# Kernel optimization log

Hardware: AMD Instinct MI355X
Metric: run time of the kernel (lower is better)

## Reference

```python
import jax, jax.numpy as jnp
import numpy as np

E, M, T, H, V = 512, 1024, 1024, 512, 10000
B, S, L = 16, 80, 200
K = 10  # pooling kernel


def avgpool2d(x, k):
    # torch AvgPool2d(k) on a 3D tensor [B, S, C]: pools over (S, C) with stride k, floor mode
    b, s, c = x.shape
    return x[:, :(s // k) * k, :(c // k) * k].reshape(b, s // k, k, c // k, k).mean(axis=(2, 4))


def lstm(x, h0, c0, Wih, Whh, bih, bhh):
    # torch single-layer LSTM, gate order (i, f, g, o); x: [B, T, H]
    def step(carry, xt):
        h, c = carry
        g = xt @ Wih.T + h @ Whh.T + bih + bhh  # [B, 4H]
        i, f, gg, o = jnp.split(g, 4, axis=-1)
        c = jax.nn.sigmoid(f) * c + jax.nn.sigmoid(i) * jnp.tanh(gg)
        h = jax.nn.sigmoid(o) * jnp.tanh(c)
        return (h, c), h
    (hT, cT), ys = jax.lax.scan(step, (h0, c0), jnp.swapaxes(x, 0, 1))
    return jnp.swapaxes(ys, 0, 1), (hT, cT)


def attend(emb, feats, lens, Ws, bs, hdim):
    # additive score: Linear(cat(emb, feat)) = emb@We.T + feat@Wf.T + b, masked softmax over valid feats
    we, wf = Ws[:, :hdim], Ws[:, hdim:]
    scores = emb @ we.T + jnp.swapaxes(feats @ wf.T, 1, 2) + bs  # [B, S, L]
    mask = jnp.arange(feats.shape[1])[None, None, :] < lens[:, None, None]
    w = jax.nn.softmax(jnp.where(mask, scores, -jnp.inf), axis=-1)
    return jnp.einsum('bsl,blf->bsf', w, feats)


def setup_inputs():
    key = jax.random.key(0)
    ks = jax.random.split(key, 30)
    n = lambda k, shape: jax.random.normal(k, shape, dtype=jnp.float32)
    p = lambda k, shape: 0.02 * jax.random.normal(k, shape, dtype=jnp.float32)
    inp = {
        'mfeat': n(ks[0], (B, L, M)),
        'tfeat': n(ks[1], (B, L, T)),
        'att_motion': n(ks[2], (B, S, M)),
        'att_tempo': n(ks[3], (B, S, T)),
        'embeddings': n(ks[4], (B, S, E)),
        'motion_batch_lens': jax.random.randint(ks[5], (B,), 100, L + 1, dtype=jnp.int32),
        'temp_batch_lens': jax.random.randint(ks[6], (B,), 100, L + 1, dtype=jnp.int32),
        'seq_batch_lens': jnp.full((B,), S, dtype=jnp.int32),
        'Wm': p(ks[7], (M, M)), 'bm': p(ks[8], (M,)),
        'Wt': p(ks[9], (T, T)), 'bt': p(ks[10], (T,)),
        'Wmm': p(ks[11], (H, E + T + M)), 'bmm': p(ks[12], (H,)),
        'Wli': p(ks[13], (H, T // K + M // K)), 'bli': p(ks[14], (H,)),
        'Wih': p(ks[15], (4 * H, H)), 'Whh': p(ks[16], (4 * H, H)),
        'bih': p(ks[17], (4 * H,)), 'bhh': p(ks[18], (4 * H,)),
        'Wsm': p(ks[19], (1, H + M)), 'bsm': p(ks[20], (1,)),
        'Wst': p(ks[21], (1, H + T)), 'bst': p(ks[22], (1,)),
        'Wo': p(ks[23], (V, H + T + M)), 'bo': p(ks[24], (V,)),
    }
    return inp


def reference(mfeat, tfeat, att_motion, att_tempo, embeddings,
              motion_batch_lens, temp_batch_lens, seq_batch_lens,
              Wm, bm, Wt, bt, Wmm, bmm, Wli, bli,
              Wih, Whh, bih, bhh, Wsm, bsm, Wst, bst, Wo, bo):
    # self-gated feature transforms
    temp_mout = att_motion @ Wm.T + bm
    temp_tout = att_tempo @ Wt.T + bt
    temp_mout = temp_mout * jax.nn.softmax(temp_mout, axis=-1)
    temp_tout = temp_tout * jax.nn.softmax(temp_tout, axis=-1)
    # multimodal fusion (dropout = identity in eval)
    mm_inp = jnp.concatenate((embeddings, temp_tout, temp_mout), axis=2)
    mm_out = mm_inp @ Wmm.T + bmm  # [B, S, H]
    # pooled init sequence -> LSTM init hidden
    mean_feat = jnp.concatenate((avgpool2d(att_tempo, K), avgpool2d(att_motion, K)), axis=2)
    m0 = mean_feat @ Wli.T + bli  # [B, S//K, H]
    z = jnp.zeros((att_motion.shape[0], H), dtype=mm_out.dtype)
    _, (h0, c0) = lstm(m0, z, z, Wih, Whh, bih, bhh)
    out, _ = lstm(mm_out, h0, c0, Wih, Whh, bih, bhh)
    act = jnp.tanh(out)
    # ragged additive attention over variable-length video features
    att_m2 = attend(act, mfeat, motion_batch_lens, Wsm, bsm, H)
    att_t2 = attend(act, tfeat, temp_batch_lens, Wst, bst, H)
    final = jnp.concatenate((act, att_t2, att_m2), axis=2) @ Wo.T + bo
    return jax.nn.log_softmax(final, axis=2)
```

## Files before the change

kernel.cpp:

```cpp
#include <hip/hip_runtime.h>
#include <hip/hip_bf16.h>
#include <math.h>


typedef __bf16 bf16x8 __attribute__((ext_vector_type(8)));
typedef float f32x4 __attribute__((ext_vector_type(4)));
typedef unsigned short u16x8 __attribute__((ext_vector_type(8)));

__device__ inline unsigned short f2b(float f){
  union { float f; unsigned u; } v; v.f = f;
  unsigned u = v.u;
  u += 0x7fff + ((u >> 16) & 1);
  return (unsigned short)(u >> 16);
}
__device__ inline float b2f(unsigned short u){
  union { unsigned u; float f; } v; v.u = (unsigned)u << 16; return v.f;
}
__device__ inline float sigm(float x){ return 1.f/(1.f + __expf(-x)); }
__device__ inline float tanh_fast(float x){
  float e = __expf(2.f*x);
  return 1.f - 2.f/(e + 1.f);
}
__device__ inline float wred_max(float v){ for (int o=32;o;o>>=1) v = fmaxf(v, __shfl_xor(v,o)); return v; }
__device__ inline float wred_sum(float v){ for (int o=32;o;o>>=1) v += __shfl_xor(v,o); return v; }

__device__ inline float bred_max(float v, float* sm){
  v = wred_max(v);
  int w = threadIdx.x >> 6;
  if ((threadIdx.x & 63) == 0) sm[w] = v;
  __syncthreads();
  v = fmaxf(fmaxf(sm[0], sm[1]), fmaxf(sm[2], sm[3]));
  __syncthreads();
  return v;
}
__device__ inline float bred_sum(float v, float* sm){
  v = wred_sum(v);
  int w = threadIdx.x >> 6;
  if ((threadIdx.x & 63) == 0) sm[w] = v;
  __syncthreads();
  v = sm[0] + sm[1] + sm[2] + sm[3];
  __syncthreads();
  return v;
}

#define GLOAD_LDS16(g, l) __builtin_amdgcn_global_load_lds( \
    (const __attribute__((address_space(1))) void*)(g), \
    (__attribute__((address_space(3))) void*)(l), 16, 0, 0)

__global__ void zero_kernel(int* p, int n){
  int i = blockIdx.x*64 + threadIdx.x;
  if (i < n) p[i] = 0;
}

__global__ void cvt7_kernel(
    const float* __restrict__ attm, const float* __restrict__ attt,
    const float* __restrict__ Wm,   const float* __restrict__ Wt,
    const float* __restrict__ Wmm,  const float* __restrict__ Wih,
    const float* __restrict__ emb,
    unsigned short* __restrict__ attm_bf, unsigned short* __restrict__ attt_bf,
    unsigned short* __restrict__ Wm_bf,   unsigned short* __restrict__ Wt_bf,
    unsigned short* __restrict__ Wmm_bf,  unsigned short* __restrict__ Wih_bf,
    unsigned short* __restrict__ mm_inp_bf)
{
  int i = blockIdx.x*256 + threadIdx.x;
  const float* s; unsigned short* d; int o;
  if (i < 458752){
    if (i < 163840){ s = attm; d = attm_bf; o = i; }
    else if (i < 327680){ s = attt; d = attt_bf; o = i - 163840; }
    else { s = Wm; d = Wm_bf; o = i - 327680; }
  } else if (i < 753664){
    if (i < 589824){ s = Wt; d = Wt_bf; o = i - 458752; }
    else { s = Wmm; d = Wmm_bf; o = i - 589824; }
  } else {
    if (i < 884736){ s = Wih; d = Wih_bf; o = i - 753664; }
    else { s = emb; d = mm_inp_bf; o = i - 884736; }
  }
  f32x4 a = ((const f32x4*)s)[(size_t)o*2];
  f32x4 b = ((const f32x4*)s)[(size_t)o*2+1];
  u16x8 v;
  v[0]=f2b(a[0]); v[1]=f2b(a[1]); v[2]=f2b(a[2]); v[3]=f2b(a[3]);
  v[4]=f2b(b[0]); v[5]=f2b(b[1]); v[6]=f2b(b[2]); v[7]=f2b(b[3]);
  if (i >= 884736){
    int row = o >> 6, c8 = (o & 63) << 3;
    *(u16x8*)&d[(size_t)row*2560 + c8] = v;
  } else {
    ((u16x8*)d)[o] = v;
  }
}

__device__ __forceinline__ void gemm_body(
    const unsigned short* __restrict__ A, const unsigned short* __restrict__ B,
    const float* __restrict__ bias1, const float* __restrict__ bias2,
    float* __restrict__ C, unsigned short* __restrict__ Cbf, int N, int K,
    unsigned short* lA, unsigned short* lB, int r0, int n0)
{
  int tid = threadIdx.x;
  int w = tid >> 6, lane = tid & 63;
  int wr = (w >> 1) << 6, wc = (w & 1) << 6;
  int lm = lane & 15, lq = lane >> 4;
  f32x4 acc[4][4] = {};

  int row0 = tid >> 2, row1 = (tid + 256) >> 2, cc = (tid & 3) << 3;
  const unsigned short* Ag0 = A + (size_t)(r0 + row0)*K + cc;
  const unsigned short* Ag1 = A + (size_t)(r0 + row1)*K + cc;
  int br0 = n0 + row0; if (br0 >= N) br0 = N - 1;
  int br1 = n0 + row1; if (br1 >= N) br1 = N - 1;
  const unsigned short* Bg0 = B + (size_t)br0*K + cc;
  const unsigned short* Bg1 = B + (size_t)br1*K + cc;
  unsigned lb0 = (unsigned)(tid & ~63) * 8;
  unsigned lb1 = 2048 + lb0;

  for (int k0 = 0; k0 < K; k0 += 32){
    GLOAD_LDS16(Ag0 + k0, &lA[lb0]);
    GLOAD_LDS16(Ag1 + k0, &lA[lb1]);
    GLOAD_LDS16(Bg0 + k0, &lB[lb0]);
    GLOAD_LDS16(Bg1 + k0, &lB[lb1]);
    __syncthreads();
    bf16x8 af[4], bfr[4];
#pragma unroll
    for (int i=0;i<4;i++){
      af[i]  = *(const bf16x8*)&lA[(wr + i*16 + lm)*32 + lq*8];
      bfr[i] = *(const bf16x8*)&lB[(wc + i*16 + lm)*32 + lq*8];
    }
#pragma unroll
    for (int i=0;i<4;i++)
#pragma unroll
      for (int j=0;j<4;j++)
        acc[i][j] = __builtin_amdgcn_mfma_f32_16x16x32_bf16(af[i], bfr[j], acc[i][j], 0, 0, 0);
    __syncthreads();
  }
#pragma unroll
  for (int i=0;i<4;i++){
    int rbase = r0 + wr + i*16 + lq*4;
#pragma unroll
    for (int j=0;j<4;j++){
      int n = n0 + wc + j*16 + lm;
      if (n < N){
        float bv = (bias1 ? bias1[n] : 0.f) + (bias2 ? bias2[n] : 0.f);
        if (Cbf){
#pragma unroll
          for (int rr=0;rr<4;rr++)
            Cbf[(size_t)(rbase + rr)*N + n] = f2b(acc[i][j][rr] + bv);
        } else {
#pragma unroll
          for (int rr=0;rr<4;rr++)
            C[(size_t)(rbase + rr)*N + n] = acc[i][j][rr] + bv;
        }
      }
    }
  }
}

__global__ __launch_bounds__(256) void gemm_bb_kernel(
    const unsigned short* __restrict__ A, const unsigned short* __restrict__ B,
    const float* __restrict__ bias1, const float* __restrict__ bias2,
    float* __restrict__ C, unsigned short* __restrict__ Cbf, int N, int K)
{
  __shared__ unsigned short lA[128*32];
  __shared__ unsigned short lB[128*32];
  gemm_body(A, B, bias1, bias2, C, Cbf, N, K, lA, lB, blockIdx.x << 7, blockIdx.y << 7);
}

__global__ __launch_bounds__(256) void gemm_bb2_kernel(
    const unsigned short* __restrict__ A0, const unsigned short* __restrict__ B0,
    const float* __restrict__ b0, float* __restrict__ C0,
    const unsigned short* __restrict__ A1, const unsigned short* __restrict__ B1,
    const float* __restrict__ b1, float* __restrict__ C1, int N, int K)
{
  __shared__ unsigned short lA[128*32];
  __shared__ unsigned short lB[128*32];
  if (blockIdx.z == 0) gemm_body(A0, B0, b0, nullptr, C0, nullptr, N, K, lA, lB, blockIdx.x << 7, blockIdx.y << 7);
  else                 gemm_body(A1, B1, b1, nullptr, C1, nullptr, N, K, lA, lB, blockIdx.x << 7, blockIdx.y << 7);
}

__global__ __launch_bounds__(256) void gemm_x12_kernel(
    const unsigned short* __restrict__ m0_bf, const unsigned short* __restrict__ mmo_bf,
    const unsigned short* __restrict__ Wih_bf,
    const float* __restrict__ bih, const float* __restrict__ bhh,
    float* __restrict__ X1, float* __restrict__ X2)
{
  __shared__ unsigned short lA[128*32];
  __shared__ unsigned short lB[128*32];
  if (blockIdx.x == 0)
    gemm_body(m0_bf, Wih_bf, bih, bhh, X1, nullptr, 2048, 512, lA, lB, 0, blockIdx.y << 7);
  else
    gemm_body(mmo_bf, Wih_bf, bih, bhh, X2, nullptr, 2048, 512, lA, lB, (blockIdx.x - 1) << 7, blockIdx.y << 7);
}

__global__ __launch_bounds__(256) void rowsmx2_kernel(const float* __restrict__ X0,
    const float* __restrict__ X1, unsigned short* __restrict__ out)
{
  __shared__ float sm[4];
  int bx = blockIdx.x, tid = threadIdx.x;
  int row = (bx < 1280) ? bx : bx - 1280;
  const float* xr = ((bx < 1280) ? X0 : X1) + (size_t)row * 1024;
  int ooff = (bx < 1280) ? 1536 : 512;
  float x[4];
#pragma unroll
  for (int j=0;j<4;j++) x[j] = xr[j*256 + tid];
  float m = fmaxf(fmaxf(x[0],x[1]), fmaxf(x[2],x[3]));
  m = bred_max(m, sm);
  float s = 0.f;
#pragma unroll
  for (int j=0;j<4;j++) s += __expf(x[j]-m);
  s = bred_sum(s, sm);
  float inv = 1.f / s;
  unsigned short* o = out + (size_t)row*2560 + ooff;
#pragma unroll
  for (int j=0;j<4;j++) o[j*256 + tid] = f2b(x[j] * (__expf(x[j]-m) * inv));
}

__global__ __launch_bounds__(256) void m0fused_kernel(
    const float* __restrict__ tempo, const float* __restrict__ motion,
    const float* __restrict__ Wli, const float* __restrict__ bli,
    unsigned short* __restrict__ m0_bf)
{
  __shared__ float rowv[204];
  int bx = blockIdx.x, tid = threadIdx.x;
  int b = bx >> 3, s = bx & 7;
  if (tid < 204){
    int c = tid;
    const float* src = (c < 102) ? (tempo  + ((size_t)(b*80 + s*10))*1024 + c*10)
                                 : (motion + ((size_t)(b*80 + s*10))*1024 + (c-102)*10);
    float acc = 0.f;
    for (int r=0;r<10;r++){
      const float* p = src + (size_t)r*1024;
#pragma unroll
      for (int cc=0;cc<10;cc++) acc += p[cc];
    }
    rowv[c] = acc * 0.01f;
  }
  __syncthreads();
  for (int c = tid; c < 512; c += 256){
    const float* w = Wli + (size_t)c*204;
    float acc = bli[c];
    for (int k=0;k<204;k++) acc += rowv[k]*w[k];
    m0_bf[(size_t)bx*512 + c] = f2b(acc);
  }
}

#define LSTM_NBLK 32
#define HP 520

__global__ __launch_bounds__(256) void lstm_fused_kernel(
    const float* __restrict__ X1, const float* __restrict__ X2,
    const float* __restrict__ Whh,
    unsigned long long* __restrict__ hb0, unsigned long long* __restrict__ hb1,
    unsigned short* __restrict__ finalA_bf,
    int* __restrict__ bar,
    const float* __restrict__ Wo, unsigned short* __restrict__ Wo_bf,
    const float* __restrict__ mfeat, const float* __restrict__ tfeat,
    const float* __restrict__ Wsm, const float* __restrict__ Wst,
    float* __restrict__ f_m, float* __restrict__ f_t)
{
  __shared__ unsigned short w_lds[64*HP];
  __shared__ unsigned short h_lds[16*HP];
  __shared__ float gb[4][16][16];
  __shared__ unsigned short hstage[16][16];
  int tid = threadIdx.x, j = blockIdx.x;

  if (j >= LSTM_NBLK){
    int hb = j - LSTM_NBLK;
    int lane = tid & 63;
    int wv = hb*4 + (tid >> 6);
    for (int r = wv; r < 6400; r += 896){
      const float* a = (r < 3200) ? (mfeat + (size_t)r*1024) : (tfeat + (size_t)(r-3200)*1024);
      const float* wvec = (r < 3200) ? (Wsm + 512) : (Wst + 512);
      float acc = 0.f;
      for (int c = lane; c < 1024; c += 64) acc += a[c]*wvec[c];
      acc = wred_sum(acc);
      if (lane == 0){ if (r < 3200) f_m[r] = acc; else f_t[r-3200] = acc; }
      __builtin_amdgcn_s_sleep(32);
    }
    const f32x4* wp = (const f32x4*)Wo;
    for (int ch = hb*256 + tid; ch < 3200000; ch += 224*256){
      f32x4 a = __builtin_nontemporal_load(wp + (size_t)ch*2);
      f32x4 b = __builtin_nontemporal_load(wp + (size_t)ch*2 + 1);
      u16x8 o;
      o[0]=f2b(a[0]); o[1]=f2b(a[1]); o[2]=f2b(a[2]); o[3]=f2b(a[3]);
      o[4]=f2b(b[0]); o[5]=f2b(b[1]); o[6]=f2b(b[2]); o[7]=f2b(b[3]);
      ((u16x8*)Wo_bf)[ch] = o;
      __builtin_amdgcn_s_sleep(127);
    }
    return;
  }

  int j16 = j*16;
  int lane = tid & 63, w = tid >> 6;
  int lm = lane & 15, lq = lane >> 4;

  for (int i = 0; i < 16; i++){
    int ch = tid + i*256;
    int r = ch >> 6, c8 = (ch & 63) << 3;
    int grow = (r >> 4)*512 + j16 + (r & 15);
    const float* s = Whh + (size_t)grow*512 + c8;
    f32x4 a = ((const f32x4*)s)[0], b = ((const f32x4*)s)[1];
    u16x8 o;
    o[0]=f2b(a[0]); o[1]=f2b(a[1]); o[2]=f2b(a[2]); o[3]=f2b(a[3]);
    o[4]=f2b(b[0]); o[5]=f2b(b[1]); o[6]=f2b(b[2]); o[7]=f2b(b[3]);
    *(u16x8*)&w_lds[r*HP + c8] = o;
  }

  float c_reg = 0.f;
  int ul = tid & 15, bb = tid >> 4;
  unsigned long long* hbufs[2] = { hb0, hb1 };
  const int wbase = ((w << 4) + lm)*HP;
  const int abase = lm*HP;
  const int koff = lq << 3;
  int sc = 0;

  for (int seg = 0; seg < 2; seg++){
    const float* Xp = seg ? X2 : X1;
    int Tst = seg ? 80 : 8;
    for (int t = 0; t < Tst; t++){
      if (sc > 0){
        if (tid == 0){
          while (__hip_atomic_load(&bar[sc-1], __ATOMIC_RELAXED, __HIP_MEMORY_SCOPE_AGENT) < LSTM_NBLK)
            __builtin_amdgcn_s_sleep(1);
        }
        __syncthreads();
      }
      size_t xrow = ((size_t)bb*Tst + t)*2048 + j16 + ul;
      float xi = Xp[xrow];
      float xf = Xp[xrow + 512];
      float xg = Xp[xrow + 1024];
      float xo = Xp[xrow + 1536];
      if (sc == 0){
        u16x8 z = {0,0,0,0,0,0,0,0};
        for (int i = tid; i < 1024; i += 256){
          int b = i >> 6, c8 = (i & 63) << 3;
          *(u16x8*)&h_lds[b*HP + c8] = z;
        }
      } else {
        const unsigned long long* src = hbufs[sc & 1];
#pragma unroll
        for (int it = 0; it < 8; it++){
          int i = tid + it*256;
          int b = i >> 7, c64 = i & 127;
          unsigned long long v = __hip_atomic_load(&src[i], __ATOMIC_RELAXED, __HIP_MEMORY_SCOPE_AGENT);
          *(unsigned long long*)&h_lds[b*HP + (c64 << 2)] = v;
        }
      }
      __syncthreads();
      f32x4 a0 = {0.f,0.f,0.f,0.f}, a1 = {0.f,0.f,0.f,0.f};
#pragma unroll
      for (int k0 = 0; k0 < 512; k0 += 64){
        bf16x8 ha = *(const bf16x8*)&h_lds[abase + k0 + koff];
        bf16x8 wa = *(const bf16x8*)&w_lds[wbase + k0 + koff];
        a0 = __builtin_amdgcn_mfma_f32_16x16x32_bf16(ha, wa, a0, 0, 0, 0);
        bf16x8 hbf = *(const bf16x8*)&h_lds[abase + k0 + 32 + koff];
        bf16x8 wbf = *(const bf16x8*)&w_lds[wbase + k0 + 32 + koff];
        a1 = __builtin_amdgcn_mfma_f32_16x16x32_bf16(hbf, wbf, a1, 0, 0, 0);
      }
      f32x4 acc = a0 + a1;
      *(f32x4*)&gb[w][lm][lq << 2] = acc;
      __syncthreads();
      float iv = gb[0][ul][bb] + xi;
      float fv = gb[1][ul][bb] + xf;
      float gv = gb[2][ul][bb] + xg;
      float ov = gb[3][ul][bb] + xo;
      c_reg = sigm(fv)*c_reg + sigm(iv)*tanh_fast(gv);
      float hn = sigm(ov)*tanh_fast(c_reg);
      hstage[bb][ul] = f2b(hn);
      __syncthreads();
      if (tid < 64){
        int b = tid >> 2, ch = tid & 3;
        unsigned long long v = *(const unsigned long long*)&hstage[b][ch << 2];
        unsigned long long* dst = hbufs[(sc + 1) & 1] + (size_t)b*128 + (j << 2) + ch;
        __hip_atomic_store(dst, v, __ATOMIC_RELAXED, __HIP_MEMORY_SCOPE_AGENT);
      }
      sc++;
      __syncthreads();
      if (tid == 0)
        __hip_atomic_fetch_add(&bar[sc-1], 1, __ATOMIC_RELAXED, __HIP_MEMORY_SCOPE_AGENT);
      if (seg)
        finalA_bf[(size_t)(bb*80 + t)*2560 + j16 + ul] = f2b(tanh_fast(hn));
    }
  }
}

__global__ __launch_bounds__(256) void attscore_kernel(
    const unsigned short* __restrict__ finalA_bf,
    const float* __restrict__ Wsm, const float* __restrict__ bsm,
    const float* __restrict__ Wst, const float* __restrict__ bst,
    const float* __restrict__ f_m, const float* __restrict__ f_t,
    const int* __restrict__ lens_m, const int* __restrict__ lens_t,
    float* __restrict__ w_m, float* __restrict__ w_t)
{
  __shared__ float sm[4];
  int bx = blockIdx.x, tid = threadIdx.x;
  bool mside = bx >= 1280;
  int row = mside ? bx - 1280 : bx;
  const float* wv = mside ? Wsm : Wst;
  float bias = (mside ? bsm : bst)[0];
  const float* f = mside ? f_m : f_t;
  const int* lens = mside ? lens_m : lens_t;
  float* w = mside ? w_m : w_t;
  const unsigned short* a = finalA_bf + (size_t)row*2560;
  float d = b2f(a[tid])*wv[tid] + b2f(a[256+tid])*wv[256+tid];
  float e = bred_sum(d, sm) + bias;
  int b = row/80;
  int len = lens[b];
  bool ok = (tid < 200) && (tid < len);
  float val = ok ? (e + f[b*200 + tid]) : -1e30f;
  float m = bred_max(val, sm);
  float ex = ok ? __expf(val - m) : 0.f;
  float s = bred_sum(ex, sm);
  if (tid < 200) w[(size_t)row*200 + tid] = ex / s;
}

__global__ __launch_bounds__(256) void attapply_kernel(
    const float* __restrict__ w_t, const float* __restrict__ w_m,
    const float* __restrict__ tfeat, const float* __restrict__ mfeat,
    unsigned short* __restrict__ finalA_bf)
{
  __shared__ float lw[8][200];
  int b = blockIdx.x, sg = blockIdx.y, z = blockIdx.z;
  const float* w = z ? w_m : w_t;
  const float* feats = z ? mfeat : tfeat;
  int coloff = z ? 1536 : 512;
  int tid = threadIdx.x;
  for (int i = tid; i < 1600; i += 256){
    int ss = i / 200, l = i - ss*200;
    lw[ss][l] = w[(size_t)(b*80 + sg*8 + ss)*200 + l];
  }
  __syncthreads();
  float4 acc[8];
#pragma unroll
  for (int s=0;s<8;s++) acc[s] = make_float4(0,0,0,0);
  const float* fb = feats + (size_t)b*200*1024 + tid*4;
  for (int l=0;l<200;l++){
    float4 v = *(const float4*)(fb + (size_t)l*1024);
#pragma unroll
    for (int s=0;s<8;s++){
      float wv = lw[s][l];
      acc[s].x += wv*v.x; acc[s].y += wv*v.y; acc[s].z += wv*v.z; acc[s].w += wv*v.w;
    }
  }
#pragma unroll
  for (int s=0;s<8;s++){
    ushort4 o;
    o.x = f2b(acc[s].x); o.y = f2b(acc[s].y); o.z = f2b(acc[s].z); o.w = f2b(acc[s].w);
    *(ushort4*)&finalA_bf[(size_t)(b*80 + sg*8 + s)*2560 + coloff + tid*4] = o;
  }
}

__global__ __launch_bounds__(256) void logsmax_kernel(float* __restrict__ out)
{
  __shared__ float buf[10000];
  __shared__ float sm[4];
  int row = blockIdx.x, tid = threadIdx.x;
  float* o = out + (size_t)row * 10000;
  float m = -1e30f;
  for (int i = tid; i < 10000; i += 256){ float v = o[i]; buf[i] = v; m = fmaxf(m, v); }
  m = bred_max(m, sm);
  float s = 0.f;
  for (int i = tid; i < 10000; i += 256) s += __expf(buf[i] - m);
  s = bred_sum(s, sm);
  float lse = m + __logf(s);
  for (int i = tid; i < 10000; i += 256) o[i] = buf[i] - lse;
}

extern "C" void kernel_launch(void* const* d_in, const int* in_sizes, int n_in,
                              void* d_out, int out_size, void* d_ws, size_t ws_size,
                              hipStream_t stream)
{
  const float* mfeat = (const float*)d_in[0];
  const float* tfeat = (const float*)d_in[1];
  const float* attm  = (const float*)d_in[2];
  const float* attt  = (const float*)d_in[3];
  const float* emb   = (const float*)d_in[4];
  const int* lens_m  = (const int*)d_in[5];
  const int* lens_t  = (const int*)d_in[6];
  const float* Wm  = (const float*)d_in[8];
  const float* bm  = (const float*)d_in[9];
  const float* Wt  = (const float*)d_in[10];
  const float* bt  = (const float*)d_in[11];
  const float* Wmm = (const float*)d_in[12];
  const float* bmm = (const float*)d_in[13];
  const float* Wli = (const float*)d_in[14];
  const float* bli = (const float*)d_in[15];
  const float* Wih = (const float*)d_in[16];
  const float* Whh = (const float*)d_in[17];
  const float* bih = (const float*)d_in[18];
  const float* bhh = (const float*)d_in[19];
  const float* Wsm = (const float*)d_in[20];
  const float* bsm = (const float*)d_in[21];
  const float* Wst = (const float*)d_in[22];
  const float* bst = (const float*)d_in[23];
  const float* Wo  = (const float*)d_in[24];
  const float* bo  = (const float*)d_in[25];
  float* out = (float*)d_out;

  char* ws = (char*)d_ws;
  size_t off = 0;
  auto alloc = [&](size_t bytes)->void* {
    void* p = (void*)(ws + off);
    off += (bytes + 255) & ~(size_t)255;
    return p;
  };
  float* moutp  = (float*)alloc(1280UL*1024*4);
  float* toutp  = (float*)alloc(1280UL*1024*4);
  float* X1     = (float*)alloc(128UL*2048*4);
  float* X2     = (float*)alloc(1280UL*2048*4);
  float* f_m = (float*)alloc(3200UL*4); float* f_t = (float*)alloc(3200UL*4);
  float* w_m = (float*)alloc(1280UL*200*4); float* w_t = (float*)alloc(1280UL*200*4);
  int* bar = (int*)alloc(128*4);
  unsigned long long* hbuf0 = (unsigned long long*)alloc(16UL*128*8);
  unsigned long long* hbuf1 = (unsigned long long*)alloc(16UL*128*8);
  unsigned short* attm_bf   = (unsigned short*)alloc(1280UL*1024*2);
  unsigned short* attt_bf   = (unsigned short*)alloc(1280UL*1024*2);
  unsigned short* Wm_bf     = (unsigned short*)alloc(1024UL*1024*2);
  unsigned short* Wt_bf     = (unsigned short*)alloc(1024UL*1024*2);
  unsigned short* Wmm_bf    = (unsigned short*)alloc(512UL*2560*2);
  unsigned short* Wih_bf    = (unsigned short*)alloc(2048UL*512*2);
  unsigned short* Wo_bf     = (unsigned short*)alloc(10000UL*2560*2);
  unsigned short* mm_inp_bf = (unsigned short*)alloc(1280UL*2560*2);
  unsigned short* mm_out_bf = (unsigned short*)alloc(1280UL*512*2);
  unsigned short* m0_bf     = (unsigned short*)alloc(128UL*512*2);
  unsigned short* finalA_bf = (unsigned short*)alloc(1280UL*2560*2);

  cvt7_kernel<<<3776, 256, 0, stream>>>(attm, attt, Wm, Wt, Wmm, Wih, emb,
      attm_bf, attt_bf, Wm_bf, Wt_bf, Wmm_bf, Wih_bf, mm_inp_bf);
  zero_kernel<<<2, 64, 0, stream>>>(bar, 128);

  gemm_bb2_kernel<<<dim3(10, 8, 2), 256, 0, stream>>>(
      attm_bf, Wm_bf, bm, moutp, attt_bf, Wt_bf, bt, toutp, 1024, 1024);
  rowsmx2_kernel<<<2560, 256, 0, stream>>>(moutp, toutp, mm_inp_bf);
  gemm_bb_kernel<<<dim3(10, 4), 256, 0, stream>>>(mm_inp_bf, Wmm_bf, bmm, nullptr,
      nullptr, mm_out_bf, 512, 2560);
  m0fused_kernel<<<128, 256, 0, stream>>>(attt, attm, Wli, bli, m0_bf);
  gemm_x12_kernel<<<dim3(11, 16), 256, 0, stream>>>(m0_bf, mm_out_bf, Wih_bf, bih, bhh, X1, X2);
  lstm_fused_kernel<<<256, 256, 0, stream>>>(X1, X2, Whh, hbuf0, hbuf1,
      finalA_bf, bar, Wo, Wo_bf, mfeat, tfeat, Wsm, Wst, f_m, f_t);
  attscore_kernel<<<2560, 256, 0, stream>>>(finalA_bf, Wsm, bsm, Wst, bst,
      f_m, f_t, lens_m, lens_t, w_m, w_t);
  attapply_kernel<<<dim3(16, 10, 2), 256, 0, stream>>>(w_t, w_m, tfeat, mfeat, finalA_bf);
  gemm_bb_kernel<<<dim3(10, 79), 256, 0, stream>>>(finalA_bf, Wo_bf, bo, nullptr,
      out, nullptr, 10000, 2560);
  logsmax_kernel<<<1280, 256, 0, stream>>>(out);
}
```

Baseline: 932.8 us.

## Move Wo bf16 conversion into upfront convert kernel and fold barrier zeroing

```diff
diff --git a/kernel.cpp b/kernel.cpp
--- a/kernel.cpp
+++ b/kernel.cpp
@@ -47,22 +47,30 @@
     (const __attribute__((address_space(1))) void*)(g), \
     (__attribute__((address_space(3))) void*)(l), 16, 0, 0)
 
-__global__ void zero_kernel(int* p, int n){
-  int i = blockIdx.x*64 + threadIdx.x;
-  if (i < n) p[i] = 0;
-}
-
-__global__ void cvt7_kernel(
+__global__ void cvt8_kernel(
     const float* __restrict__ attm, const float* __restrict__ attt,
     const float* __restrict__ Wm,   const float* __restrict__ Wt,
     const float* __restrict__ Wmm,  const float* __restrict__ Wih,
-    const float* __restrict__ emb,
+    const float* __restrict__ emb,  const float* __restrict__ Wo,
     unsigned short* __restrict__ attm_bf, unsigned short* __restrict__ attt_bf,
     unsigned short* __restrict__ Wm_bf,   unsigned short* __restrict__ Wt_bf,
     unsigned short* __restrict__ Wmm_bf,  unsigned short* __restrict__ Wih_bf,
-    unsigned short* __restrict__ mm_inp_bf)
+    unsigned short* __restrict__ mm_inp_bf, unsigned short* __restrict__ Wo_bf,
+    int* __restrict__ bar)
 {
   int i = blockIdx.x*256 + threadIdx.x;
+  if (blockIdx.x == 0 && threadIdx.x < 128) bar[threadIdx.x] = 0;
+  if (i >= 966656){
+    int o = i - 966656;
+    const f32x4* wp = (const f32x4*)Wo;
+    f32x4 a = __builtin_nontemporal_load(wp + (size_t)o*2);
+    f32x4 b = __builtin_nontemporal_load(wp + (size_t)o*2 + 1);
+    u16x8 v;
+    v[0]=f2b(a[0]); v[1]=f2b(a[1]); v[2]=f2b(a[2]); v[3]=f2b(a[3]);
+    v[4]=f2b(b[0]); v[5]=f2b(b[1]); v[6]=f2b(b[2]); v[7]=f2b(b[3]);
+    ((u16x8*)Wo_bf)[o] = v;
+    return;
+  }
   const float* s; unsigned short* d; int o;
   if (i < 458752){
     if (i < 163840){ s = attm; d = attm_bf; o = i; }
@@ -248,7 +256,6 @@
     unsigned long long* __restrict__ hb0, unsigned long long* __restrict__ hb1,
     unsigned short* __restrict__ finalA_bf,
     int* __restrict__ bar,
-    const float* __restrict__ Wo, unsigned short* __restrict__ Wo_bf,
     const float* __restrict__ mfeat, const float* __restrict__ tfeat,
     const float* __restrict__ Wsm, const float* __restrict__ Wst,
     float* __restrict__ f_m, float* __restrict__ f_t)
@@ -270,17 +277,6 @@
       for (int c = lane; c < 1024; c += 64) acc += a[c]*wvec[c];
       acc = wred_sum(acc);
       if (lane == 0){ if (r < 3200) f_m[r] = acc; else f_t[r-3200] = acc; }
-      __builtin_amdgcn_s_sleep(32);
-    }
-    const f32x4* wp = (const f32x4*)Wo;
-    for (int ch = hb*256 + tid; ch < 3200000; ch += 224*256){
-      f32x4 a = __builtin_nontemporal_load(wp + (size_t)ch*2);
-      f32x4 b = __builtin_nontemporal_load(wp + (size_t)ch*2 + 1);
-      u16x8 o;
-      o[0]=f2b(a[0]); o[1]=f2b(a[1]); o[2]=f2b(a[2]); o[3]=f2b(a[3]);
-      o[4]=f2b(b[0]); o[5]=f2b(b[1]); o[6]=f2b(b[2]); o[7]=f2b(b[3]);
-      ((u16x8*)Wo_bf)[ch] = o;
-      __builtin_amdgcn_s_sleep(127);
     }
     return;
   }
@@ -520,9 +516,8 @@
   unsigned short* m0_bf     = (unsigned short*)alloc(128UL*512*2);
   unsigned short* finalA_bf = (unsigned short*)alloc(1280UL*2560*2);
 
-  cvt7_kernel<<<3776, 256, 0, stream>>>(attm, attt, Wm, Wt, Wmm, Wih, emb,
-      attm_bf, attt_bf, Wm_bf, Wt_bf, Wmm_bf, Wih_bf, mm_inp_bf);
-  zero_kernel<<<2, 64, 0, stream>>>(bar, 128);
+  cvt8_kernel<<<16276, 256, 0, stream>>>(attm, attt, Wm, Wt, Wmm, Wih, emb, Wo,
+      attm_bf, attt_bf, Wm_bf, Wt_bf, Wmm_bf, Wih_bf, mm_inp_bf, Wo_bf, bar);
 
   gemm_bb2_kernel<<<dim3(10, 8, 2), 256, 0, stream>>>(
       attm_bf, Wm_bf, bm, moutp, attt_bf, Wt_bf, bt, toutp, 1024, 1024);
@@ -532,7 +527,7 @@
   m0fused_kernel<<<128, 256, 0, stream>>>(attt, attm, Wli, bli, m0_bf);
   gemm_x12_kernel<<<dim3(11, 16), 256, 0, stream>>>(m0_bf, mm_out_bf, Wih_bf, bih, bhh, X1, X2);
   lstm_fused_kernel<<<256, 256, 0, stream>>>(X1, X2, Whh, hbuf0, hbuf1,
-      finalA_bf, bar, Wo, Wo_bf, mfeat, tfeat, Wsm, Wst, f_m, f_t);
+      finalA_bf, bar, mfeat, tfeat, Wsm, Wst, f_m, f_t);
   attscore_kernel<<<2560, 256, 0, stream>>>(finalA_bf, Wsm, bsm, Wst, bst,
       f_m, f_t, lens_m, lens_t, w_m, w_t);
   attapply_kernel<<<dim3(16, 10, 2), 256, 0, stream>>>(w_t, w_m, tfeat, mfeat, finalA_bf);
```

Result: slower. 954.8 us (+2.4%).

## Fold zero/m0 kernels into convert kernel, move feat-score work into GEMM launch

Applied to the files above, without the earlier changes.

```diff
diff --git a/kernel.cpp b/kernel.cpp
--- a/kernel.cpp
+++ b/kernel.cpp
@@ -47,12 +47,7 @@
     (const __attribute__((address_space(1))) void*)(g), \
     (__attribute__((address_space(3))) void*)(l), 16, 0, 0)
 
-__global__ void zero_kernel(int* p, int n){
-  int i = blockIdx.x*64 + threadIdx.x;
-  if (i < n) p[i] = 0;
-}
-
-__global__ void cvt7_kernel(
+__global__ void cvt7m_kernel(
     const float* __restrict__ attm, const float* __restrict__ attt,
     const float* __restrict__ Wm,   const float* __restrict__ Wt,
     const float* __restrict__ Wmm,  const float* __restrict__ Wih,
@@ -60,9 +55,37 @@
     unsigned short* __restrict__ attm_bf, unsigned short* __restrict__ attt_bf,
     unsigned short* __restrict__ Wm_bf,   unsigned short* __restrict__ Wt_bf,
     unsigned short* __restrict__ Wmm_bf,  unsigned short* __restrict__ Wih_bf,
-    unsigned short* __restrict__ mm_inp_bf)
-{
+    unsigned short* __restrict__ mm_inp_bf,
+    const float* __restrict__ Wli, const float* __restrict__ bli,
+    unsigned short* __restrict__ m0_bf, int* __restrict__ bar)
+{
+  if (blockIdx.x >= 3776){
+    __shared__ float rowv[204];
+    int bx = blockIdx.x - 3776, tid = threadIdx.x;
+    int b = bx >> 3, s = bx & 7;
+    if (tid < 204){
+      int c = tid;
+      const float* src = (c < 102) ? (attt + ((size_t)(b*80 + s*10))*1024 + c*10)
+                                   : (attm + ((size_t)(b*80 + s*10))*1024 + (c-102)*10);
+      float acc = 0.f;
+      for (int r=0;r<10;r++){
+        const float* p = src + (size_t)r*1024;
+#pragma unroll
+        for (int cc=0;cc<10;cc++) acc += p[cc];
+      }
+      rowv[c] = acc * 0.01f;
+    }
+    __syncthreads();
+    for (int c = tid; c < 512; c += 256){
+      const float* w = Wli + (size_t)c*204;
+      float acc = bli[c];
+      for (int k=0;k<204;k++) acc += rowv[k]*w[k];
+      m0_bf[(size_t)bx*512 + c] = f2b(acc);
+    }
+    return;
+  }
   int i = blockIdx.x*256 + threadIdx.x;
+  if (blockIdx.x == 0 && threadIdx.x < 128) bar[threadIdx.x] = 0;
   const float* s; unsigned short* d; int o;
   if (i < 458752){
     if (i < 163840){ s = attm; d = attm_bf; o = i; }
@@ -161,16 +184,30 @@
   gemm_body(A, B, bias1, bias2, C, Cbf, N, K, lA, lB, blockIdx.x << 7, blockIdx.y << 7);
 }
 
-__global__ __launch_bounds__(256) void gemm_bb2_kernel(
+__global__ __launch_bounds__(256) void gemm_bb2f_kernel(
     const unsigned short* __restrict__ A0, const unsigned short* __restrict__ B0,
     const float* __restrict__ b0, float* __restrict__ C0,
     const unsigned short* __restrict__ A1, const unsigned short* __restrict__ B1,
-    const float* __restrict__ b1, float* __restrict__ C1, int N, int K)
+    const float* __restrict__ b1, float* __restrict__ C1, int N, int K,
+    const float* __restrict__ mfeat, const float* __restrict__ tfeat,
+    const float* __restrict__ Wsm, const float* __restrict__ Wst,
+    float* __restrict__ f_m, float* __restrict__ f_t)
 {
   __shared__ unsigned short lA[128*32];
   __shared__ unsigned short lB[128*32];
-  if (blockIdx.z == 0) gemm_body(A0, B0, b0, nullptr, C0, nullptr, N, K, lA, lB, blockIdx.x << 7, blockIdx.y << 7);
-  else                 gemm_body(A1, B1, b1, nullptr, C1, nullptr, N, K, lA, lB, blockIdx.x << 7, blockIdx.y << 7);
+  if (blockIdx.z == 0){ gemm_body(A0, B0, b0, nullptr, C0, nullptr, N, K, lA, lB, blockIdx.x << 7, blockIdx.y << 7); return; }
+  if (blockIdx.z == 1){ gemm_body(A1, B1, b1, nullptr, C1, nullptr, N, K, lA, lB, blockIdx.x << 7, blockIdx.y << 7); return; }
+  int flat = blockIdx.x*8 + blockIdx.y;
+  int lane = threadIdx.x & 63;
+  int wv = flat*4 + (threadIdx.x >> 6);
+  for (int r = wv; r < 6400; r += 320){
+    const float* a = (r < 3200) ? (mfeat + (size_t)r*1024) : (tfeat + (size_t)(r-3200)*1024);
+    const float* wvec = (r < 3200) ? (Wsm + 512) : (Wst + 512);
+    float acc = 0.f;
+    for (int c = lane; c < 1024; c += 64) acc += a[c]*wvec[c];
+    acc = wred_sum(acc);
+    if (lane == 0){ if (r < 3200) f_m[r] = acc; else f_t[r-3200] = acc; }
+  }
 }
 
 __global__ __launch_bounds__(256) void gemm_x12_kernel(
@@ -210,35 +247,6 @@
   for (int j=0;j<4;j++) o[j*256 + tid] = f2b(x[j] * (__expf(x[j]-m) * inv));
 }
 
-__global__ __launch_bounds__(256) void m0fused_kernel(
-    const float* __restrict__ tempo, const float* __restrict__ motion,
-    const float* __restrict__ Wli, const float* __restrict__ bli,
-    unsigned short* __restrict__ m0_bf)
-{
-  __shared__ float rowv[204];
-  int bx = blockIdx.x, tid = threadIdx.x;
-  int b = bx >> 3, s = bx & 7;
-  if (tid < 204){
-    int c = tid;
-    const float* src = (c < 102) ? (tempo  + ((size_t)(b*80 + s*10))*1024 + c*10)
-                                 : (motion + ((size_t)(b*80 + s*10))*1024 + (c-102)*10);
-    float acc = 0.f;
-    for (int r=0;r<10;r++){
-      const float* p = src + (size_t)r*1024;
-#pragma unroll
-      for (int cc=0;cc<10;cc++) acc += p[cc];
-    }
-    rowv[c] = acc * 0.01f;
-  }
-  __syncthreads();
-  for (int c = tid; c < 512; c += 256){
-    const float* w = Wli + (size_t)c*204;
-    float acc = bli[c];
-    for (int k=0;k<204;k++) acc += rowv[k]*w[k];
-    m0_bf[(size_t)bx*512 + c] = f2b(acc);
-  }
-}
-
 #define LSTM_NBLK 32
 #define HP 520
 
@@ -248,10 +256,7 @@
     unsigned long long* __restrict__ hb0, unsigned long long* __restrict__ hb1,
     unsigned short* __restrict__ finalA_bf,
     int* __restrict__ bar,
-    const float* __restrict__ Wo, unsigned short* __restrict__ Wo_bf,
-    const float* __restrict__ mfeat, const float* __restrict__ tfeat,
-    const float* __restrict__ Wsm, const float* __restrict__ Wst,
-    float* __restrict__ f_m, float* __restrict__ f_t)
+    const float* __restrict__ Wo, unsigned short* __restrict__ Wo_bf)
 {
   __shared__ unsigned short w_lds[64*HP];
   __shared__ unsigned short h_lds[16*HP];
@@ -261,17 +266,6 @@
 
   if (j >= LSTM_NBLK){
     int hb = j - LSTM_NBLK;
-    int lane = tid & 63;
-    int wv = hb*4 + (tid >> 6);
-    for (int r = wv; r < 6400; r += 896){
-      const float* a = (r < 3200) ? (mfeat + (size_t)r*1024) : (tfeat + (size_t)(r-3200)*1024);
-      const float* wvec = (r < 3200) ? (Wsm + 512) : (Wst + 512);
-      float acc = 0.f;
-      for (int c = lane; c < 1024; c += 64) acc += a[c]*wvec[c];
-      acc = wred_sum(acc);
-      if (lane == 0){ if (r < 3200) f_m[r] = acc; else f_t[r-3200] = acc; }
-      __builtin_amdgcn_s_sleep(32);
-    }
     const f32x4* wp = (const f32x4*)Wo;
     for (int ch = hb*256 + tid; ch < 3200000; ch += 224*256){
       f32x4 a = __builtin_nontemporal_load(wp + (size_t)ch*2);
@@ -280,7 +274,6 @@
       o[0]=f2b(a[0]); o[1]=f2b(a[1]); o[2]=f2b(a[2]); o[3]=f2b(a[3]);
       o[4]=f2b(b[0]); o[5]=f2b(b[1]); o[6]=f2b(b[2]); o[7]=f2b(b[3]);
       ((u16x8*)Wo_bf)[ch] = o;
-      __builtin_amdgcn_s_sleep(127);
     }
     return;
   }
@@ -447,18 +440,17 @@
 
 __global__ __launch_bounds__(256) void logsmax_kernel(float* __restrict__ out)
 {
-  __shared__ float buf[10000];
   __shared__ float sm[4];
   int row = blockIdx.x, tid = threadIdx.x;
   float* o = out + (size_t)row * 10000;
   float m = -1e30f;
-  for (int i = tid; i < 10000; i += 256){ float v = o[i]; buf[i] = v; m = fmaxf(m, v); }
+  for (int i = tid; i < 10000; i += 256) m = fmaxf(m, o[i]);
   m = bred_max(m, sm);
   float s = 0.f;
-  for (int i = tid; i < 10000; i += 256) s += __expf(buf[i] - m);
+  for (int i = tid; i < 10000; i += 256) s += __expf(o[i] - m);
   s = bred_sum(s, sm);
   float lse = m + __logf(s);
-  for (int i = tid; i < 10000; i += 256) o[i] = buf[i] - lse;
+  for (int i = tid; i < 10000; i += 256) o[i] = o[i] - lse;
 }
 
 extern "C" void kernel_launch(void* const* d_in, const int* in_sizes, int n_in,
@@ -520,19 +512,19 @@
   unsigned short* m0_bf     = (unsigned short*)alloc(128UL*512*2);
   unsigned short* finalA_bf = (unsigned short*)alloc(1280UL*2560*2);
 
-  cvt7_kernel<<<3776, 256, 0, stream>>>(attm, attt, Wm, Wt, Wmm, Wih, emb,
-      attm_bf, attt_bf, Wm_bf, Wt_bf, Wmm_bf, Wih_bf, mm_inp_bf);
-  zero_kernel<<<2, 64, 0, stream>>>(bar, 128);
-
-  gemm_bb2_kernel<<<dim3(10, 8, 2), 256, 0, stream>>>(
-      attm_bf, Wm_bf, bm, moutp, attt_bf, Wt_bf, bt, toutp, 1024, 1024);
+  cvt7m_kernel<<<3904, 256, 0, stream>>>(attm, attt, Wm, Wt, Wmm, Wih, emb,
+      attm_bf, attt_bf, Wm_bf, Wt_bf, Wmm_bf, Wih_bf, mm_inp_bf,
+      Wli, bli, m0_bf, bar);
+
+  gemm_bb2f_kernel<<<dim3(10, 8, 3), 256, 0, stream>>>(
+      attm_bf, Wm_bf, bm, moutp, attt_bf, Wt_bf, bt, toutp, 1024, 1024,
+      mfeat, tfeat, Wsm, Wst, f_m, f_t);
   rowsmx2_kernel<<<2560, 256, 0, stream>>>(moutp, toutp, mm_inp_bf);
   gemm_bb_kernel<<<dim3(10, 4), 256, 0, stream>>>(mm_inp_bf, Wmm_bf, bmm, nullptr,
       nullptr, mm_out_bf, 512, 2560);
-  m0fused_kernel<<<128, 256, 0, stream>>>(attt, attm, Wli, bli, m0_bf);
   gemm_x12_kernel<<<dim3(11, 16), 256, 0, stream>>>(m0_bf, mm_out_bf, Wih_bf, bih, bhh, X1, X2);
   lstm_fused_kernel<<<256, 256, 0, stream>>>(X1, X2, Whh, hbuf0, hbuf1,
-      finalA_bf, bar, Wo, Wo_bf, mfeat, tfeat, Wsm, Wst, f_m, f_t);
+      finalA_bf, bar, Wo, Wo_bf);
   attscore_kernel<<<2560, 256, 0, stream>>>(finalA_bf, Wsm, bsm, Wst, bst,
       f_m, f_t, lens_m, lens_t, w_m, w_t);
   attapply_kernel<<<dim3(16, 10, 2), 256, 0, stream>>>(w_t, w_m, tfeat, mfeat, finalA_bf);
```

After: 1.067 ms. +14.3%, slower.
